# Kernel tuning notes

Hardware: AMD Instinct MI355X
Metric: run time of the kernel (lower is better)

## Reference

```python
import jax, jax.numpy as jnp
import numpy as np

N = 20000      # nodes (single node type)
E = 320000     # edges per relation (avg degree 16)
R = 3          # relations / edge types
L = 3          # layers
H = 4          # heads
D = 64         # dim per head (hid_size // n_heads)
IN = 256       # in_size == hid_size
OUT = 128      # out_size
NEG_SLOPE = 0.2


def setup_inputs() -> dict:
    key = jax.random.key(0)
    ks = jax.random.split(key, 8)
    x = jax.random.normal(ks[0], (N, IN), jnp.float32)
    edge_src = jax.random.randint(ks[1], (R, E), 0, N, dtype=jnp.int32)
    edge_dst = jax.random.randint(ks[2], (R, E), 0, N, dtype=jnp.int32)
    W = jax.random.normal(ks[3], (L, R, IN, H * D), jnp.float32) * (1.0 / np.sqrt(IN))
    attn_l = jax.random.normal(ks[4], (L, R, H, D), jnp.float32) * 0.1
    attn_r = jax.random.normal(ks[5], (L, R, H, D), jnp.float32) * 0.1
    bias = jnp.zeros((L, R, H * D), jnp.float32)
    fc_w = jax.random.normal(ks[6], (IN, OUT), jnp.float32) * (1.0 / np.sqrt(IN))
    fc_b = jnp.zeros((OUT,), jnp.float32)
    return dict(x=x, edge_src=edge_src, edge_dst=edge_dst, W=W,
                attn_l=attn_l, attn_r=attn_r, bias=bias, fc_w=fc_w, fc_b=fc_b)


def _gat_conv(h, src, dst, W_r, al, ar, b_r):
    # h: [N, IN] -> feat: [N, H, D]
    feat = (h @ W_r).reshape(N, H, D)
    el = jnp.sum(feat * al, axis=-1)                      # [N, H]
    er = jnp.sum(feat * ar, axis=-1)                      # [N, H]
    e = jax.nn.leaky_relu(el[src] + er[dst], NEG_SLOPE)   # [E, H]
    # segment softmax over incoming edges of each dst node, per head
    m = jax.ops.segment_max(e, dst, num_segments=N)       # [N, H]
    a = jnp.exp(e - m[dst])
    s = jax.ops.segment_sum(a, dst, num_segments=N)       # [N, H]
    alpha = a / s[dst]                                    # [E, H]
    # weighted scatter-add of source features: [N, H, D]
    out = jax.ops.segment_sum(alpha[:, :, None] * feat[src], dst, num_segments=N)
    return out + b_r.reshape(1, H, D)


def reference(x, edge_src, edge_dst, W, attn_l, attn_r, bias, fc_w, fc_b):
    h = x
    for l in range(L):
        acc = jnp.zeros((N, H, D), h.dtype)
        for r in range(R):  # sum-aggregate across relations (HeteroGraphConv aggregate='sum')
            acc = acc + _gat_conv(h, edge_src[r], edge_dst[r],
                                  W[l, r], attn_l[l, r], attn_r[l, r], bias[l, r])
        h = acc.reshape(N, H * D)
        if l != L - 1:
            h = jax.nn.relu(h)  # dropout = identity in eval
    return h @ fc_w + fc_b  # [N, OUT]
```

## Files before the change

### kernel.cpp

```cpp
#include <hip/hip_runtime.h>
#include <math.h>

#define NN 20000
#define EE 320000
#define RR 3
#define LL 3
#define HH 4
#define DD 64
#define CDIM 256
#define OUTD 128
#define NEG 0.2f

typedef float f32x4 __attribute__((ext_vector_type(4)));
typedef short sh8 __attribute__((ext_vector_type(8)));

__device__ __forceinline__ ushort f2bf(float f) {
    union { float f; uint u; } v; v.f = f;
    uint r = (v.u + 0x7FFF + ((v.u >> 16) & 1)) >> 16;
    return (ushort)r;
}
__device__ __forceinline__ float bf2f(ushort u) {
    union { uint u; float f; } v; v.u = ((uint)u) << 16;
    return v.f;
}
__device__ __forceinline__ float bflo(uint p) { return bf2f((ushort)(p & 0xffff)); }
__device__ __forceinline__ float bfhi(uint p) { return bf2f((ushort)(p >> 16)); }


__global__ void zero_ints(int* p, int n) {
    int i = blockIdx.x * blockDim.x + threadIdx.x;
    if (i < n) p[i] = 0;
}

__global__ void count_deg(const int* __restrict__ edge_dst, int* __restrict__ deg) {
    int i = blockIdx.x * blockDim.x + threadIdx.x;
    if (i >= RR * EE) return;
    int r = i / EE;
    atomicAdd(&deg[r * NN + edge_dst[i]], 1);
}

__global__ __launch_bounds__(1024) void scan_kernel(
    const int* __restrict__ deg, int* __restrict__ row_ptr) {
    int r = blockIdx.x;
    const int* d = deg + r * NN;
    int* rp = row_ptr + r * (NN + 1);
    __shared__ int wsum[16];
    int lane = threadIdx.x & 63, wv = threadIdx.x >> 6;
    if (threadIdx.x == 0) rp[0] = 0;
    int carry = 0;
    for (int base = 0; base < NN; base += 1024) {
        int i = base + threadIdx.x;
        int v = (i < NN) ? d[i] : 0;
        int s = v;
        #pragma unroll
        for (int off = 1; off < 64; off <<= 1) {
            int n = __shfl_up(s, off, 64);
            if (lane >= off) s += n;
        }
        if (lane == 63) wsum[wv] = s;
        __syncthreads();
        if (wv == 0) {
            int ws = (lane < 16) ? wsum[lane] : 0;
            #pragma unroll
            for (int off = 1; off < 16; off <<= 1) {
                int n = __shfl_up(ws, off, 64);
                if (lane >= off) ws += n;
            }
            if (lane < 16) wsum[lane] = ws;
        }
        __syncthreads();
        int incl = carry + (wv ? wsum[wv - 1] : 0) + s;
        if (i < NN) rp[i + 1] = incl;
        carry += wsum[15];
        __syncthreads();
    }
}

__global__ void fill_csr(const int* __restrict__ edge_src, const int* __restrict__ edge_dst,
                         int* __restrict__ cursor, int* __restrict__ csr_src) {
    int i = blockIdx.x * blockDim.x + threadIdx.x;
    if (i >= RR * EE) return;
    int r = i / EE;
    int dst = edge_dst[i];
    int pos = atomicAdd(&cursor[r * (NN + 1) + dst], 1);
    csr_src[r * EE + pos] = edge_src[i];
}


__global__ void cvt_bf16x4(const float* __restrict__ in, ushort* __restrict__ out, int n4) {
    int i = blockIdx.x * blockDim.x + threadIdx.x;
    if (i >= n4) return;
    float4 v = *(const float4*)(in + (size_t)i * 4);
    ushort4 o;
    o.x = f2bf(v.x); o.y = f2bf(v.y); o.z = f2bf(v.z); o.w = f2bf(v.w);
    *(ushort4*)(out + (size_t)i * 4) = o;
}

__global__ void prep_Wt(const float* __restrict__ W, ushort* __restrict__ Wt, int K, int N) {
    __shared__ float tile[32][33];
    int kb = blockIdx.x * 32, nb = blockIdx.y * 32;
    size_t base = (size_t)blockIdx.z * K * N;
    for (int yy = threadIdx.y; yy < 32; yy += 8)
        tile[yy][threadIdx.x] = W[base + (size_t)(kb + yy) * N + nb + threadIdx.x];
    __syncthreads();
    for (int yy = threadIdx.y; yy < 32; yy += 8)
        Wt[base + (size_t)(nb + yy) * K + kb + threadIdx.x] = f2bf(tile[threadIdx.x][yy]);
}


#define TM 128
#define TN 128
#define TK 32
#define LP 40

__global__ __launch_bounds__(256) void gemm_bf16(
    const ushort* __restrict__ A, const ushort* __restrict__ Bt0, void* __restrict__ C0,
    int M, int K, int Ncol, long strideB, long strideC,
    const float* __restrict__ bias, int out_fp32,
    const float* __restrict__ al_all, const float* __restrict__ ar_all,
    float* __restrict__ el_all, float* __restrict__ er_all) {
    __shared__ alignas(16) ushort As[TM * LP];
    __shared__ alignas(16) ushort Bs[TN * LP];
    const ushort* Bt = Bt0 + (size_t)blockIdx.z * strideB;
    int m0 = blockIdx.x * TM, n0 = blockIdx.y * TN;
    int t = threadIdx.x;
    int wave = t >> 6, lane = t & 63;
    int q = lane >> 4, l16 = lane & 15;
    int wrow = (wave >> 1) * 64, wcol = (wave & 1) * 64;

    f32x4 acc[4][4];
    #pragma unroll
    for (int i = 0; i < 4; i++)
        #pragma unroll
        for (int j = 0; j < 4; j++)
            #pragma unroll
            for (int k = 0; k < 4; k++) acc[i][j][k] = 0.f;

    for (int k0 = 0; k0 < K; k0 += TK) {
        #pragma unroll
        for (int s = 0; s < 2; s++) {
            int qid = t + s * 256;
            int row = qid >> 2, kq = (qid & 3) * 8;
            uint4 v = make_uint4(0, 0, 0, 0);
            int gr = m0 + row;
            if (gr < M) v = *(const uint4*)(A + (size_t)gr * K + k0 + kq);
            *(uint4*)(As + row * LP + kq) = v;
        }
        #pragma unroll
        for (int s = 0; s < 2; s++) {
            int qid = t + s * 256;
            int row = qid >> 2, kq = (qid & 3) * 8;
            uint4 v = *(const uint4*)(Bt + (size_t)(n0 + row) * K + k0 + kq);
            *(uint4*)(Bs + row * LP + kq) = v;
        }
        __syncthreads();
        sh8 af[4], bfr[4];
        #pragma unroll
        for (int i = 0; i < 4; i++)
            af[i] = *(const sh8*)(As + (wrow + i * 16 + l16) * LP + q * 8);
        #pragma unroll
        for (int j = 0; j < 4; j++)
            bfr[j] = *(const sh8*)(Bs + (wcol + j * 16 + l16) * LP + q * 8);
        #pragma unroll
        for (int i = 0; i < 4; i++)
            #pragma unroll
            for (int j = 0; j < 4; j++)
                acc[i][j] = __builtin_amdgcn_mfma_f32_16x16x32_bf16(af[i], bfr[j], acc[i][j], 0, 0, 0);
        __syncthreads();
    }

    if (out_fp32) {
        float* C = (float*)C0 + (size_t)blockIdx.z * strideC;
        #pragma unroll
        for (int i = 0; i < 4; i++) {
            #pragma unroll
            for (int reg = 0; reg < 4; reg++) {
                int row = m0 + wrow + i * 16 + q * 4 + reg;
                if (row >= M) continue;
                #pragma unroll
                for (int j = 0; j < 4; j++) {
                    int col = n0 + wcol + j * 16 + l16;
                    float v = acc[i][j][reg];
                    if (bias) v += bias[col];
                    C[(size_t)row * Ncol + col] = v;
                }
            }
        }
    } else {
        ushort* C = (ushort*)C0 + (size_t)blockIdx.z * strideC;
        #pragma unroll
        for (int i = 0; i < 4; i++) {
            #pragma unroll
            for (int reg = 0; reg < 4; reg++) {
                int row = m0 + wrow + i * 16 + q * 4 + reg;
                if (row >= M) continue;
                #pragma unroll
                for (int j = 0; j < 4; j++) {
                    int col = n0 + wcol + j * 16 + l16;
                    C[(size_t)row * Ncol + col] = f2bf(acc[i][j][reg]);
                }
            }
        }
    }

    if (el_all) {
        const float* al = al_all + (size_t)blockIdx.z * CDIM;
        const float* ar = ar_all + (size_t)blockIdx.z * CDIM;
        float* elp = el_all + (size_t)blockIdx.z * NN * HH;
        float* erp = er_all + (size_t)blockIdx.z * NN * HH;
        int head = (n0 + wcol) >> 6;
        float alj[4], arj[4];
        #pragma unroll
        for (int j = 0; j < 4; j++) {
            int gcol = n0 + wcol + j * 16 + l16;
            alj[j] = al[gcol];
            arj[j] = ar[gcol];
        }
        #pragma unroll
        for (int i = 0; i < 4; i++) {
            #pragma unroll
            for (int reg = 0; reg < 4; reg++) {
                int row = m0 + wrow + i * 16 + q * 4 + reg;
                float pl = 0.f, pr = 0.f;
                #pragma unroll
                for (int j = 0; j < 4; j++) {
                    pl = fmaf(acc[i][j][reg], alj[j], pl);
                    pr = fmaf(acc[i][j][reg], arj[j], pr);
                }
                #pragma unroll
                for (int m = 1; m < 16; m <<= 1) {
                    pl += __shfl_xor(pl, m, 64);
                    pr += __shfl_xor(pr, m, 64);
                }
                if (l16 == 0 && row < M) {
                    elp[(size_t)row * HH + head] = pl;
                    erp[(size_t)row * HH + head] = pr;
                }
            }
        }
    }
}

__global__ __launch_bounds__(256) void aggregate_fused(
    const ushort* __restrict__ feat16, const float* __restrict__ el,
    const float* __restrict__ er, const int* __restrict__ row_ptr,
    const int* __restrict__ csr_src, const float* __restrict__ bias,
    ushort* __restrict__ hout, int relu) {
    int wv = threadIdx.x >> 6, lane = threadIdx.x & 63;
    int node = blockIdx.x * 4 + wv;
    if (node >= NN) return;
    int c0 = lane * 4;
    int h = lane >> 4;
    float t0 = 0.f, t1 = 0.f, t2 = 0.f, t3 = 0.f;
    #pragma unroll
    for (int r = 0; r < RR; r++) {
        const int* rp = row_ptr + r * (NN + 1);
        int beg = rp[node], end = rp[node + 1];
        const ushort* fr = feat16 + (size_t)r * NN * CDIM;
        const float* elr = el + (size_t)r * NN * HH;
        float ern = er[((size_t)r * NN + node) * HH + h];
        const int* cs = csr_src + (size_t)r * EE;
        float p0 = 0.f, p1 = 0.f, p2 = 0.f, p3 = 0.f, ssum = 0.f;
        int e = beg;
        for (; e + 4 <= end; e += 4) {
            int s0 = cs[e], s1 = cs[e + 1], s2 = cs[e + 2], s3 = cs[e + 3];
            float x0 = elr[s0 * HH + h];
            float x1 = elr[s1 * HH + h];
            float x2 = elr[s2 * HH + h];
            float x3 = elr[s3 * HH + h];
            uint2 f0 = *(const uint2*)(fr + (size_t)s0 * CDIM + c0);
            uint2 f1 = *(const uint2*)(fr + (size_t)s1 * CDIM + c0);
            uint2 f2 = *(const uint2*)(fr + (size_t)s2 * CDIM + c0);
            uint2 f3 = *(const uint2*)(fr + (size_t)s3 * CDIM + c0);
            x0 += ern; x1 += ern; x2 += ern; x3 += ern;
            x0 = x0 > 0.f ? x0 : NEG * x0;
            x1 = x1 > 0.f ? x1 : NEG * x1;
            x2 = x2 > 0.f ? x2 : NEG * x2;
            x3 = x3 > 0.f ? x3 : NEG * x3;
            float a0 = __expf(x0), a1 = __expf(x1), a2 = __expf(x2), a3 = __expf(x3);
            ssum += a0 + a1 + a2 + a3;
            p0 = fmaf(a0, bflo(f0.x), p0); p1 = fmaf(a0, bfhi(f0.x), p1);
            p2 = fmaf(a0, bflo(f0.y), p2); p3 = fmaf(a0, bfhi(f0.y), p3);
            p0 = fmaf(a1, bflo(f1.x), p0); p1 = fmaf(a1, bfhi(f1.x), p1);
            p2 = fmaf(a1, bflo(f1.y), p2); p3 = fmaf(a1, bfhi(f1.y), p3);
            p0 = fmaf(a2, bflo(f2.x), p0); p1 = fmaf(a2, bfhi(f2.x), p1);
            p2 = fmaf(a2, bflo(f2.y), p2); p3 = fmaf(a2, bfhi(f2.y), p3);
            p0 = fmaf(a3, bflo(f3.x), p0); p1 = fmaf(a3, bfhi(f3.x), p1);
            p2 = fmaf(a3, bflo(f3.y), p2); p3 = fmaf(a3, bfhi(f3.y), p3);
        }
        for (; e < end; e++) {
            int s = cs[e];
            float x = elr[s * HH + h] + ern;
            x = x > 0.f ? x : NEG * x;
            float a = __expf(x);
            uint2 f = *(const uint2*)(fr + (size_t)s * CDIM + c0);
            ssum += a;
            p0 = fmaf(a, bflo(f.x), p0); p1 = fmaf(a, bfhi(f.x), p1);
            p2 = fmaf(a, bflo(f.y), p2); p3 = fmaf(a, bfhi(f.y), p3);
        }
        float is = (end > beg) ? 1.f / ssum : 0.f;
        t0 += p0 * is + bias[r * CDIM + c0];
        t1 += p1 * is + bias[r * CDIM + c0 + 1];
        t2 += p2 * is + bias[r * CDIM + c0 + 2];
        t3 += p3 * is + bias[r * CDIM + c0 + 3];
    }
    if (relu) {
        t0 = fmaxf(t0, 0.f); t1 = fmaxf(t1, 0.f);
        t2 = fmaxf(t2, 0.f); t3 = fmaxf(t3, 0.f);
    }
    uint2 o;
    o.x = (uint)f2bf(t0) | ((uint)f2bf(t1) << 16);
    o.y = (uint)f2bf(t2) | ((uint)f2bf(t3) << 16);
    *(uint2*)(hout + (size_t)node * CDIM + c0) = o;
}


extern "C" void kernel_launch(void* const* d_in, const int* in_sizes, int n_in,
                              void* d_out, int out_size, void* d_ws, size_t ws_size,
                              hipStream_t stream) {
    const float* x        = (const float*)d_in[0];
    const int*   edge_src = (const int*)d_in[1];
    const int*   edge_dst = (const int*)d_in[2];
    const float* W        = (const float*)d_in[3];
    const float* attn_l   = (const float*)d_in[4];
    const float* attn_r   = (const float*)d_in[5];
    const float* bias     = (const float*)d_in[6];
    const float* fc_w     = (const float*)d_in[7];
    const float* fc_b     = (const float*)d_in[8];
    float* out = (float*)d_out;

    char* ws = (char*)d_ws;
    size_t off = 0;
    auto alloc = [&](size_t bytes) {
        void* p = ws + off;
        off = (off + bytes + 255) & ~(size_t)255;
        return p;
    };
    ushort* x16    = (ushort*)alloc((size_t)NN * CDIM * 2);
    ushort* h16    = (ushort*)alloc((size_t)NN * CDIM * 2);
    ushort* feat16 = (ushort*)alloc((size_t)RR * NN * CDIM * 2);
    ushort* Wt16   = (ushort*)alloc((size_t)LL * RR * CDIM * CDIM * 2);
    ushort* fct16  = (ushort*)alloc((size_t)OUTD * CDIM * 2);
    float* el      = (float*)alloc((size_t)RR * NN * HH * 4);
    float* er      = (float*)alloc((size_t)RR * NN * HH * 4);
    int* row_ptr   = (int*)alloc((size_t)RR * (NN + 1) * 4);
    int* cursor    = (int*)alloc((size_t)RR * (NN + 1) * 4);
    int* csr_src   = (int*)alloc((size_t)RR * EE * 4);
    int* deg       = (int*)alloc((size_t)RR * NN * 4);

    zero_ints<<<dim3((RR * NN + 1023) / 1024), dim3(1024), 0, stream>>>(deg, RR * NN);
    count_deg<<<dim3((RR * EE + 255) / 256), dim3(256), 0, stream>>>(edge_dst, deg);
    scan_kernel<<<dim3(RR), dim3(1024), 0, stream>>>(deg, row_ptr);
    hipMemcpyAsync(cursor, row_ptr, (size_t)RR * (NN + 1) * 4,
                   hipMemcpyDeviceToDevice, stream);
    fill_csr<<<dim3((RR * EE + 255) / 256), dim3(256), 0, stream>>>(
        edge_src, edge_dst, cursor, csr_src);

    cvt_bf16x4<<<dim3((NN * CDIM / 4 + 255) / 256), dim3(256), 0, stream>>>(x, x16, NN * CDIM / 4);
    prep_Wt<<<dim3(CDIM / 32, CDIM / 32, LL * RR), dim3(32, 8), 0, stream>>>(W, Wt16, CDIM, CDIM);
    prep_Wt<<<dim3(CDIM / 32, OUTD / 32, 1), dim3(32, 8), 0, stream>>>(fc_w, fct16, CDIM, OUTD);

    const ushort* hin = x16;
    for (int l = 0; l < LL; l++) {
        const ushort* Wl = Wt16 + (size_t)l * RR * CDIM * CDIM;
        dim3 g((NN + TM - 1) / TM, CDIM / TN, RR);
        gemm_bf16<<<g, dim3(256), 0, stream>>>(hin, Wl, feat16, NN, CDIM, CDIM,
                                               (long)CDIM * CDIM, (long)NN * CDIM, nullptr, 0,
                                               attn_l + (size_t)l * RR * CDIM,
                                               attn_r + (size_t)l * RR * CDIM, el, er);
        aggregate_fused<<<dim3(NN / 4), dim3(256), 0, stream>>>(
            feat16, el, er, row_ptr, csr_src, bias + (size_t)l * RR * CDIM,
            h16, (l != LL - 1) ? 1 : 0);
        hin = h16;
    }
    dim3 gf((NN + TM - 1) / TM, OUTD / TN, 1);
    gemm_bf16<<<gf, dim3(256), 0, stream>>>(h16, fct16, out, NN, CDIM, OUTD,
                                            0, 0, fc_b, 1, nullptr, nullptr, nullptr, nullptr);
}
```

Measured before the change: 534.6 us.

## Load GEMM tiles via global_load_lds with XOR-swizzled LDS and merge setup kernels

The GEMM now copies A and B tiles straight from global memory into LDS with global_load_lds, skipping the trip through registers. It replaces the padded LDS layout with an XOR swizzle to avoid bank conflicts. The activation buffers are padded to 20096 rows so the row bounds check can go, though the padded rows are never zeroed and read uninitialised data that is masked only on output. Setup is also trimmed: a memset replaces the zero kernel, the scan writes the cursor copy itself, and the two weight-prep launches become one.

```diff
diff --git a/kernel.cpp b/kernel.cpp
--- a/kernel.cpp
+++ b/kernel.cpp
@@ -2,6 +2,7 @@
 #include <math.h>
 
 #define NN 20000
+#define NN_PAD 20096
 #define EE 320000
 #define RR 3
 #define LL 3
@@ -26,11 +27,12 @@
 __device__ __forceinline__ float bflo(uint p) { return bf2f((ushort)(p & 0xffff)); }
 __device__ __forceinline__ float bfhi(uint p) { return bf2f((ushort)(p >> 16)); }
 
-
-__global__ void zero_ints(int* p, int n) {
-    int i = blockIdx.x * blockDim.x + threadIdx.x;
-    if (i < n) p[i] = 0;
-}
+__device__ __forceinline__ void glds16(const ushort* g, ushort* l) {
+    __builtin_amdgcn_global_load_lds(
+        (const __attribute__((address_space(1))) void*)g,
+        (__attribute__((address_space(3))) void*)l, 16, 0, 0);
+}
+
 
 __global__ void count_deg(const int* __restrict__ edge_dst, int* __restrict__ deg) {
     int i = blockIdx.x * blockDim.x + threadIdx.x;
@@ -40,13 +42,14 @@
 }
 
 __global__ __launch_bounds__(1024) void scan_kernel(
-    const int* __restrict__ deg, int* __restrict__ row_ptr) {
+    const int* __restrict__ deg, int* __restrict__ row_ptr, int* __restrict__ cursor) {
     int r = blockIdx.x;
     const int* d = deg + r * NN;
     int* rp = row_ptr + r * (NN + 1);
+    int* cur = cursor + r * (NN + 1);
     __shared__ int wsum[16];
     int lane = threadIdx.x & 63, wv = threadIdx.x >> 6;
-    if (threadIdx.x == 0) rp[0] = 0;
+    if (threadIdx.x == 0) { rp[0] = 0; cur[0] = 0; }
     int carry = 0;
     for (int base = 0; base < NN; base += 1024) {
         int i = base + threadIdx.x;
@@ -70,7 +73,7 @@
         }
         __syncthreads();
         int incl = carry + (wv ? wsum[wv - 1] : 0) + s;
-        if (i < NN) rp[i + 1] = incl;
+        if (i < NN) { rp[i + 1] = incl; cur[i + 1] = incl; }
         carry += wsum[15];
         __syncthreads();
     }
@@ -96,22 +99,35 @@
     *(ushort4*)(out + (size_t)i * 4) = o;
 }
 
-__global__ void prep_Wt(const float* __restrict__ W, ushort* __restrict__ Wt, int K, int N) {
+__global__ void prep_all(const float* __restrict__ W, const float* __restrict__ fc_w,
+                         ushort* __restrict__ Wt, ushort* __restrict__ fct) {
     __shared__ float tile[32][33];
+    int z = blockIdx.z;
+    const float* src;
+    ushort* dst;
+    int N;
+    if (z < LL * RR) {
+        src = W + (size_t)z * CDIM * CDIM;
+        dst = Wt + (size_t)z * CDIM * CDIM;
+        N = CDIM;
+    } else {
+        src = fc_w;
+        dst = fct;
+        N = OUTD;
+    }
     int kb = blockIdx.x * 32, nb = blockIdx.y * 32;
-    size_t base = (size_t)blockIdx.z * K * N;
+    if (nb >= N) return;
     for (int yy = threadIdx.y; yy < 32; yy += 8)
-        tile[yy][threadIdx.x] = W[base + (size_t)(kb + yy) * N + nb + threadIdx.x];
+        tile[yy][threadIdx.x] = src[(size_t)(kb + yy) * N + nb + threadIdx.x];
     __syncthreads();
     for (int yy = threadIdx.y; yy < 32; yy += 8)
-        Wt[base + (size_t)(nb + yy) * K + kb + threadIdx.x] = f2bf(tile[threadIdx.x][yy]);
+        dst[(size_t)(nb + yy) * CDIM + kb + threadIdx.x] = f2bf(tile[threadIdx.x][yy]);
 }
 
 
 #define TM 128
 #define TN 128
 #define TK 32
-#define LP 40
 
 __global__ __launch_bounds__(256) void gemm_bf16(
     const ushort* __restrict__ A, const ushort* __restrict__ Bt0, void* __restrict__ C0,
@@ -119,8 +135,8 @@
     const float* __restrict__ bias, int out_fp32,
     const float* __restrict__ al_all, const float* __restrict__ ar_all,
     float* __restrict__ el_all, float* __restrict__ er_all) {
-    __shared__ alignas(16) ushort As[TM * LP];
-    __shared__ alignas(16) ushort Bs[TN * LP];
+    __shared__ alignas(16) ushort As[TM * 32];
+    __shared__ alignas(16) ushort Bs[TN * 32];
     const ushort* Bt = Bt0 + (size_t)blockIdx.z * strideB;
     int m0 = blockIdx.x * TM, n0 = blockIdx.y * TN;
     int t = threadIdx.x;
@@ -128,6 +144,16 @@
     int q = lane >> 4, l16 = lane & 15;
     int wrow = (wave >> 1) * 64, wcol = (wave & 1) * 64;
 
+    int sw = (q ^ ((l16 >> 1) & 3)) * 8;
+    int a_off[4], b_off[4];
+    #pragma unroll
+    for (int i = 0; i < 4; i++) {
+        a_off[i] = (wrow + i * 16 + l16) * 32 + sw;
+        b_off[i] = (wcol + i * 16 + l16) * 32 + sw;
+    }
+    int row_a = t >> 2;
+    int ch_a  = ((t & 3) ^ ((row_a >> 1) & 3)) * 8;
+
     f32x4 acc[4][4];
     #pragma unroll
     for (int i = 0; i < 4; i++)
@@ -140,27 +166,21 @@
         #pragma unroll
         for (int s = 0; s < 2; s++) {
             int qid = t + s * 256;
-            int row = qid >> 2, kq = (qid & 3) * 8;
-            uint4 v = make_uint4(0, 0, 0, 0);
-            int gr = m0 + row;
-            if (gr < M) v = *(const uint4*)(A + (size_t)gr * K + k0 + kq);
-            *(uint4*)(As + row * LP + kq) = v;
+            int row = row_a + s * 64;
+            glds16(A + (size_t)(m0 + row) * K + k0 + ch_a, As + qid * 8);
         }
         #pragma unroll
         for (int s = 0; s < 2; s++) {
             int qid = t + s * 256;
-            int row = qid >> 2, kq = (qid & 3) * 8;
-            uint4 v = *(const uint4*)(Bt + (size_t)(n0 + row) * K + k0 + kq);
-            *(uint4*)(Bs + row * LP + kq) = v;
+            int row = row_a + s * 64;
+            glds16(Bt + (size_t)(n0 + row) * K + k0 + ch_a, Bs + qid * 8);
         }
         __syncthreads();
         sh8 af[4], bfr[4];
         #pragma unroll
-        for (int i = 0; i < 4; i++)
-            af[i] = *(const sh8*)(As + (wrow + i * 16 + l16) * LP + q * 8);
-        #pragma unroll
-        for (int j = 0; j < 4; j++)
-            bfr[j] = *(const sh8*)(Bs + (wcol + j * 16 + l16) * LP + q * 8);
+        for (int i = 0; i < 4; i++) af[i] = *(const sh8*)(As + a_off[i]);
+        #pragma unroll
+        for (int j = 0; j < 4; j++) bfr[j] = *(const sh8*)(Bs + b_off[j]);
         #pragma unroll
         for (int i = 0; i < 4; i++)
             #pragma unroll
@@ -336,8 +356,8 @@
         off = (off + bytes + 255) & ~(size_t)255;
         return p;
     };
-    ushort* x16    = (ushort*)alloc((size_t)NN * CDIM * 2);
-    ushort* h16    = (ushort*)alloc((size_t)NN * CDIM * 2);
+    ushort* x16    = (ushort*)alloc((size_t)NN_PAD * CDIM * 2);
+    ushort* h16    = (ushort*)alloc((size_t)NN_PAD * CDIM * 2);
     ushort* feat16 = (ushort*)alloc((size_t)RR * NN * CDIM * 2);
     ushort* Wt16   = (ushort*)alloc((size_t)LL * RR * CDIM * CDIM * 2);
     ushort* fct16  = (ushort*)alloc((size_t)OUTD * CDIM * 2);
@@ -348,22 +368,20 @@
     int* csr_src   = (int*)alloc((size_t)RR * EE * 4);
     int* deg       = (int*)alloc((size_t)RR * NN * 4);
 
-    zero_ints<<<dim3((RR * NN + 1023) / 1024), dim3(1024), 0, stream>>>(deg, RR * NN);
+    hipMemsetAsync(deg, 0, (size_t)RR * NN * 4, stream);
     count_deg<<<dim3((RR * EE + 255) / 256), dim3(256), 0, stream>>>(edge_dst, deg);
-    scan_kernel<<<dim3(RR), dim3(1024), 0, stream>>>(deg, row_ptr);
-    hipMemcpyAsync(cursor, row_ptr, (size_t)RR * (NN + 1) * 4,
-                   hipMemcpyDeviceToDevice, stream);
+    scan_kernel<<<dim3(RR), dim3(1024), 0, stream>>>(deg, row_ptr, cursor);
     fill_csr<<<dim3((RR * EE + 255) / 256), dim3(256), 0, stream>>>(
         edge_src, edge_dst, cursor, csr_src);
 
     cvt_bf16x4<<<dim3((NN * CDIM / 4 + 255) / 256), dim3(256), 0, stream>>>(x, x16, NN * CDIM / 4);
-    prep_Wt<<<dim3(CDIM / 32, CDIM / 32, LL * RR), dim3(32, 8), 0, stream>>>(W, Wt16, CDIM, CDIM);
-    prep_Wt<<<dim3(CDIM / 32, OUTD / 32, 1), dim3(32, 8), 0, stream>>>(fc_w, fct16, CDIM, OUTD);
+    prep_all<<<dim3(CDIM / 32, CDIM / 32, LL * RR + 1), dim3(32, 8), 0, stream>>>(
+        W, fc_w, Wt16, fct16);
 
     const ushort* hin = x16;
     for (int l = 0; l < LL; l++) {
         const ushort* Wl = Wt16 + (size_t)l * RR * CDIM * CDIM;
-        dim3 g((NN + TM - 1) / TM, CDIM / TN, RR);
+        dim3 g(NN_PAD / TM, CDIM / TN, RR);
         gemm_bf16<<<g, dim3(256), 0, stream>>>(hin, Wl, feat16, NN, CDIM, CDIM,
                                                (long)CDIM * CDIM, (long)NN * CDIM, nullptr, 0,
                                                attn_l + (size_t)l * RR * CDIM,
@@ -373,7 +391,7 @@
             h16, (l != LL - 1) ? 1 : 0);
         hin = h16;
     }
-    dim3 gf((NN + TM - 1) / TM, OUTD / TN, 1);
+    dim3 gf(NN_PAD / TM, OUTD / TN, 1);
     gemm_bf16<<<gf, dim3(256), 0, stream>>>(h16, fct16, out, NN, CDIM, OUTD,
                                             0, 0, fc_b, 1, nullptr, nullptr, nullptr, nullptr);
 }
```

Result: faster. 513.4 us (-4.0%).
